# Performance work log

Hardware: AMD Instinct MI355X
Metric: run time of the kernel (lower is better)

## Reference

```python
import jax, jax.numpy as jnp
import numpy as np

G = 2000      # num_genes
TF = 64       # num_tf
B = 32        # batch (cells)
_peaks = 5 + (np.arange(G) % 46)          # ragged peaks per gene, avg ~27
T = int(_peaks.sum())                      # 54736 total peak columns
E = G * 16                                 # directed edges before symmetrization


def setup_inputs() -> dict:
    key = jax.random.key(0)
    ks = jax.random.split(key, 8)
    x = jax.random.normal(ks[0], (B, TF, T), jnp.float32)
    # gene id of each peak column (sorted, ragged segment structure = cut[])
    gene_ids = jnp.asarray(np.repeat(np.arange(G), _peaks), jnp.int32)
    # all per-gene subNet Linear weights flattened into one [TF, T] table
    w_sub = jax.random.normal(ks[1], (TF, T), jnp.float32) * 0.02
    b_sub = jax.random.normal(ks[2], (G,), jnp.float32) * 0.02
    rng = np.random.default_rng(1)
    src = rng.integers(0, G, E)
    dst = rng.integers(0, G, E)
    ei = np.stack([np.concatenate([src, dst]), np.concatenate([dst, src])])
    edge_index = jnp.asarray(ei, jnp.int32)                 # [2, 2E], symmetrized
    w_conv = jax.random.normal(ks[3], (1, 2), jnp.float32) * 0.5   # GCN lin weight (in=1, out=2)
    b_conv = jax.random.normal(ks[4], (2,), jnp.float32) * 0.1
    w_out = jax.random.normal(ks[5], (G * 2, 3), jnp.float32) * 0.02
    b_out = jax.random.normal(ks[6], (3,), jnp.float32) * 0.02
    return dict(x=x, gene_ids=gene_ids, w_sub=w_sub, b_sub=b_sub,
                edge_index=edge_index, w_conv=w_conv, b_conv=b_conv,
                w_out=w_out, b_out=b_out)


def reference(x, gene_ids, w_sub, b_sub, edge_index, w_conv, b_conv, w_out, b_out):
    # --- ragged per-gene subNets: Linear(num_peak_i*TF, 1) each ---
    # out[b,g] = sum_{t, p in gene g} x[b,t,p] * w[g,t,p] + b_sub[g]
    z = (x * w_sub[None]).sum(axis=1)                        # [B, T] reduce over TF
    x_cat = jnp.zeros((x.shape[0], b_sub.shape[0]), x.dtype)
    x_cat = x_cat.at[:, gene_ids].add(z) + b_sub[None]       # segment-sum over peaks
    x_cat = jax.nn.relu(x_cat)                               # cat_activate

    # --- GCNConv(1, 2, add_self_loops=False) on node features [B, G, 1] ---
    h = jnp.einsum('bn,f->bnf', x_cat, w_conv[0])            # lin: [B, G, 2]
    src, dst = edge_index[0], edge_index[1]
    deg = jnp.zeros((b_sub.shape[0],), x.dtype).at[dst].add(1.0)
    dinv = jnp.where(deg > 0, jax.lax.rsqrt(jnp.maximum(deg, 1.0)), 0.0)
    norm = dinv[src] * dinv[dst]                             # [2E]
    msg = h[:, src, :] * norm[None, :, None]                 # gather + scale
    agg = jnp.zeros_like(h).at[:, dst, :].add(msg) + b_conv  # scatter-add + bias
    g = jax.nn.relu(agg).reshape(x.shape[0], -1)             # [B, G*2]

    out = g @ w_out + b_out                                   # [B, 3]
    return x_cat, g, out
```

## Files before the change

kernel.cpp:

```cpp
#include <hip/hip_runtime.h>


__global__ void k_subnet4(const float* __restrict__ x, const float* __restrict__ w_sub,
                          const int* __restrict__ gene_ids, float* __restrict__ acc,
                          int TF, int T, int G, int B) {
    int t = (blockIdx.x * blockDim.x + threadIdx.x) * 4;
    if (t >= T) return;
    int b0 = blockIdx.y * 4;
    int nb = B - b0; if (nb > 4) nb = 4;
    const size_t planeT = (size_t)TF * T;

    if (t + 3 < T && (T % 4) == 0) {
        const size_t strideV = (size_t)T / 4;
        const float4* wp = (const float4*)(w_sub + t);
        const float4* xp0 = (const float4*)(x + (size_t)(b0 + 0) * planeT + t);
        const float4* xp1 = (const float4*)(x + (size_t)(b0 + 1) * planeT + t);
        const float4* xp2 = (const float4*)(x + (size_t)(b0 + 2) * planeT + t);
        const float4* xp3 = (const float4*)(x + (size_t)(b0 + 3) * planeT + t);

        float4 a0 = make_float4(0.f,0.f,0.f,0.f);
        float4 a1 = a0, a2 = a0, a3 = a0;

        if (nb == 4) {
            #pragma unroll 4
            for (int tf = 0; tf < TF; ++tf) {
                size_t off = (size_t)tf * strideV;
                float4 wv = wp[off];
                float4 x0 = xp0[off];
                float4 x1 = xp1[off];
                float4 x2 = xp2[off];
                float4 x3 = xp3[off];
                a0.x += x0.x*wv.x; a0.y += x0.y*wv.y; a0.z += x0.z*wv.z; a0.w += x0.w*wv.w;
                a1.x += x1.x*wv.x; a1.y += x1.y*wv.y; a1.z += x1.z*wv.z; a1.w += x1.w*wv.w;
                a2.x += x2.x*wv.x; a2.y += x2.y*wv.y; a2.z += x2.z*wv.z; a2.w += x2.w*wv.w;
                a3.x += x3.x*wv.x; a3.y += x3.y*wv.y; a3.z += x3.z*wv.z; a3.w += x3.w*wv.w;
            }
        } else {
            for (int tf = 0; tf < TF; ++tf) {
                size_t off = (size_t)tf * strideV;
                float4 wv = wp[off];
                if (nb > 0) { float4 xv = xp0[off]; a0.x += xv.x*wv.x; a0.y += xv.y*wv.y; a0.z += xv.z*wv.z; a0.w += xv.w*wv.w; }
                if (nb > 1) { float4 xv = xp1[off]; a1.x += xv.x*wv.x; a1.y += xv.y*wv.y; a1.z += xv.z*wv.z; a1.w += xv.w*wv.w; }
                if (nb > 2) { float4 xv = xp2[off]; a2.x += xv.x*wv.x; a2.y += xv.y*wv.y; a2.z += xv.z*wv.z; a2.w += xv.w*wv.w; }
            }
        }

        int g0 = gene_ids[t], g1 = gene_ids[t+1], g2 = gene_ids[t+2], g3 = gene_ids[t+3];
        float4 as[4] = {a0, a1, a2, a3};
        for (int bb = 0; bb < nb; ++bb) {
            float* base = acc + (size_t)(b0 + bb) * G;
            float4 a = as[bb];
            float v = a.x; int cg = g0;
            if (g1 == cg) v += a.y; else { atomicAdd(base + cg, v); cg = g1; v = a.y; }
            if (g2 == cg) v += a.z; else { atomicAdd(base + cg, v); cg = g2; v = a.z; }
            if (g3 == cg) v += a.w; else { atomicAdd(base + cg, v); cg = g3; v = a.w; }
            atomicAdd(base + cg, v);
        }
    } else {
        for (int bb = 0; bb < nb; ++bb) {
            int b = b0 + bb;
            for (int tt = t; tt < T && tt < t + 4; ++tt) {
                float a = 0.f;
                for (int tf = 0; tf < TF; ++tf)
                    a += x[(size_t)b * planeT + (size_t)tf * T + tt] * w_sub[(size_t)tf * T + tt];
                atomicAdd(acc + (size_t)b * G + gene_ids[tt], a);
            }
        }
    }
}

__global__ void k_xcat(const float* __restrict__ acc, const float* __restrict__ b_sub,
                       float* __restrict__ xcat, int BG, int G) {
    int i = blockIdx.x * blockDim.x + threadIdx.x;
    if (i >= BG) return;
    int g = i % G;
    float v = acc[i] + b_sub[g];
    xcat[i] = v > 0.f ? v : 0.f;
}

__global__ void k_deg(const int* __restrict__ ei, float* __restrict__ deg, int E2) {
    int e = blockIdx.x * blockDim.x + threadIdx.x;
    if (e < E2) atomicAdd(&deg[ei[E2 + e]], 1.0f);
}

__global__ void k_dinv(float* __restrict__ deg, int G) {
    int g = blockIdx.x * blockDim.x + threadIdx.x;
    if (g < G) {
        float d = deg[g];
        deg[g] = (d > 0.f) ? (1.0f / sqrtf(fmaxf(d, 1.0f))) : 0.f;
    }
}

__global__ void k_scatter(const float* __restrict__ xcat, const int* __restrict__ ei,
                          const float* __restrict__ dinv, float* __restrict__ s,
                          int G, int E2, int total) {
    int idx = blockIdx.x * blockDim.x + threadIdx.x;
    if (idx >= total) return;
    int b = idx / E2;
    int e = idx - b * E2;
    int src = ei[e], dst = ei[E2 + e];
    float norm = dinv[src] * dinv[dst];
    atomicAdd(&s[(size_t)b * G + dst], xcat[(size_t)b * G + src] * norm);
}

__global__ void k_gfin(const float* __restrict__ s, const float* __restrict__ w_conv,
                       const float* __restrict__ b_conv, float* __restrict__ gout, int BG) {
    int i = blockIdx.x * blockDim.x + threadIdx.x;
    if (i >= BG) return;
    float sv = s[i];
    float g0 = sv * w_conv[0] + b_conv[0];
    float g1 = sv * w_conv[1] + b_conv[1];
    gout[2 * (size_t)i + 0] = g0 > 0.f ? g0 : 0.f;
    gout[2 * (size_t)i + 1] = g1 > 0.f ? g1 : 0.f;
}

__global__ void k_out(const float* __restrict__ gmat, const float* __restrict__ w_out,
                      const float* __restrict__ b_out, float* __restrict__ out, int G2) {
    int b = blockIdx.x;
    float a0 = 0.f, a1 = 0.f, a2 = 0.f;
    for (int i = threadIdx.x; i < G2; i += blockDim.x) {
        float gv = gmat[(size_t)b * G2 + i];
        a0 += gv * w_out[3 * i + 0];
        a1 += gv * w_out[3 * i + 1];
        a2 += gv * w_out[3 * i + 2];
    }
    __shared__ float red[3][256];
    red[0][threadIdx.x] = a0; red[1][threadIdx.x] = a1; red[2][threadIdx.x] = a2;
    __syncthreads();
    for (int s = blockDim.x / 2; s > 0; s >>= 1) {
        if ((int)threadIdx.x < s) {
            red[0][threadIdx.x] += red[0][threadIdx.x + s];
            red[1][threadIdx.x] += red[1][threadIdx.x + s];
            red[2][threadIdx.x] += red[2][threadIdx.x + s];
        }
        __syncthreads();
    }
    if (threadIdx.x == 0) {
        out[b * 3 + 0] = red[0][0] + b_out[0];
        out[b * 3 + 1] = red[1][0] + b_out[1];
        out[b * 3 + 2] = red[2][0] + b_out[2];
    }
}

extern "C" void kernel_launch(void* const* d_in, const int* in_sizes, int n_in,
                              void* d_out, int out_size, void* d_ws, size_t ws_size,
                              hipStream_t stream) {
    const float* x        = (const float*)d_in[0];
    const int*   gene_ids = (const int*)d_in[1];
    const float* w_sub    = (const float*)d_in[2];
    const float* b_sub    = (const float*)d_in[3];
    const int*   ei       = (const int*)d_in[4];
    const float* w_conv   = (const float*)d_in[5];
    const float* b_conv   = (const float*)d_in[6];
    const float* w_out    = (const float*)d_in[7];
    const float* b_out    = (const float*)d_in[8];

    const int G  = in_sizes[3];
    const int T  = in_sizes[1];
    const int TF = in_sizes[2] / T;
    const int B  = in_sizes[0] / (TF * T);
    const int E2 = in_sizes[4] / 2;
    const int BG = B * G;
    const int G2 = 2 * G;

    float* acc = (float*)d_ws;
    float* deg = acc + BG;
    float* s   = deg + G;
    size_t zero_bytes = (size_t)(BG + G + BG) * sizeof(float);
    hipMemsetAsync(d_ws, 0, zero_bytes, stream);

    float* out_xcat = (float*)d_out;
    float* out_g    = out_xcat + BG;
    float* out_fin  = out_g + (size_t)B * G2;

    {
        int tthreads = (T + 3) / 4;
        dim3 grid((tthreads + 255) / 256, (B + 3) / 4);
        k_subnet4<<<grid, 256, 0, stream>>>(x, w_sub, gene_ids, acc, TF, T, G, B);
    }
    k_xcat<<<(BG + 255) / 256, 256, 0, stream>>>(acc, b_sub, out_xcat, BG, G);
    k_deg<<<(E2 + 255) / 256, 256, 0, stream>>>(ei, deg, E2);
    k_dinv<<<(G + 255) / 256, 256, 0, stream>>>(deg, G);
    {
        int total = B * E2;
        k_scatter<<<(total + 255) / 256, 256, 0, stream>>>(out_xcat, ei, deg, s, G, E2, total);
    }
    k_gfin<<<(BG + 255) / 256, 256, 0, stream>>>(s, w_conv, b_conv, out_g, BG);
    k_out<<<B, 256, 0, stream>>>(out_g, w_out, b_out, out_fin, G2);
}
```

Baseline: 750.0 us.

## Precompute edge norms, batch scatter over 4 cells, fuse GCN finalize with output GEMV

Edge normalisation is computed once per edge into a workspace buffer. The scatter kernel now processes four batch rows per thread, so edge indices and the norm are reused across cells. The GCN bias/ReLU finalize is fused with the output projection into one per-batch kernel, which removes a launch and a re-read of g. The norm buffer sits past the zeroed region and needs extra workspace, and the single-block-per-batch fused kernel has low parallelism.

```diff
diff --git a/kernel.cpp b/kernel.cpp
--- a/kernel.cpp
+++ b/kernel.cpp
@@ -1,9 +1,10 @@
 #include <hip/hip_runtime.h>
 
 
-__global__ void k_subnet4(const float* __restrict__ x, const float* __restrict__ w_sub,
-                          const int* __restrict__ gene_ids, float* __restrict__ acc,
-                          int TF, int T, int G, int B) {
+__global__ __launch_bounds__(256) void k_subnet4(
+        const float* __restrict__ x, const float* __restrict__ w_sub,
+        const int* __restrict__ gene_ids, float* __restrict__ acc,
+        int TF, int T, int G, int B) {
     int t = (blockIdx.x * blockDim.x + threadIdx.x) * 4;
     if (t >= T) return;
     int b0 = blockIdx.y * 4;
@@ -12,7 +13,7 @@
 
     if (t + 3 < T && (T % 4) == 0) {
         const size_t strideV = (size_t)T / 4;
-        const float4* wp = (const float4*)(w_sub + t);
+        const float4* wp  = (const float4*)(w_sub + t);
         const float4* xp0 = (const float4*)(x + (size_t)(b0 + 0) * planeT + t);
         const float4* xp1 = (const float4*)(x + (size_t)(b0 + 1) * planeT + t);
         const float4* xp2 = (const float4*)(x + (size_t)(b0 + 2) * planeT + t);
@@ -91,54 +92,61 @@
     }
 }
 
-__global__ void k_scatter(const float* __restrict__ xcat, const int* __restrict__ ei,
-                          const float* __restrict__ dinv, float* __restrict__ s,
-                          int G, int E2, int total) {
-    int idx = blockIdx.x * blockDim.x + threadIdx.x;
-    if (idx >= total) return;
-    int b = idx / E2;
-    int e = idx - b * E2;
-    int src = ei[e], dst = ei[E2 + e];
-    float norm = dinv[src] * dinv[dst];
-    atomicAdd(&s[(size_t)b * G + dst], xcat[(size_t)b * G + src] * norm);
+__global__ void k_norm(const int* __restrict__ ei, const float* __restrict__ dinv,
+                       float* __restrict__ norm, int E2) {
+    int e = blockIdx.x * blockDim.x + threadIdx.x;
+    if (e < E2) norm[e] = dinv[ei[e]] * dinv[ei[E2 + e]];
 }
 
-__global__ void k_gfin(const float* __restrict__ s, const float* __restrict__ w_conv,
-                       const float* __restrict__ b_conv, float* __restrict__ gout, int BG) {
-    int i = blockIdx.x * blockDim.x + threadIdx.x;
-    if (i >= BG) return;
-    float sv = s[i];
-    float g0 = sv * w_conv[0] + b_conv[0];
-    float g1 = sv * w_conv[1] + b_conv[1];
-    gout[2 * (size_t)i + 0] = g0 > 0.f ? g0 : 0.f;
-    gout[2 * (size_t)i + 1] = g1 > 0.f ? g1 : 0.f;
+__global__ void k_scatter4(const float* __restrict__ xcat, const int* __restrict__ ei,
+                           const float* __restrict__ norm, float* __restrict__ s,
+                           int G, int E2, int B) {
+    int e = blockIdx.x * blockDim.x + threadIdx.x;
+    if (e >= E2) return;
+    int b0 = blockIdx.y * 4;
+    int nb = B - b0; if (nb > 4) nb = 4;
+    int src = ei[e], dst = ei[E2 + e];
+    float nm = norm[e];
+    for (int bb = 0; bb < nb; ++bb) {
+        size_t row = (size_t)(b0 + bb) * G;
+        atomicAdd(&s[row + dst], xcat[row + src] * nm);
+    }
 }
 
-__global__ void k_out(const float* __restrict__ gmat, const float* __restrict__ w_out,
-                      const float* __restrict__ b_out, float* __restrict__ out, int G2) {
+__global__ void k_gout(const float* __restrict__ s, const float* __restrict__ w_conv,
+                       const float* __restrict__ b_conv, const float* __restrict__ w_out,
+                       const float* __restrict__ b_out, float* __restrict__ gout,
+                       float* __restrict__ outfin, int G) {
     int b = blockIdx.x;
+    float wc0 = w_conv[0], wc1 = w_conv[1];
+    float bc0 = b_conv[0], bc1 = b_conv[1];
     float a0 = 0.f, a1 = 0.f, a2 = 0.f;
-    for (int i = threadIdx.x; i < G2; i += blockDim.x) {
-        float gv = gmat[(size_t)b * G2 + i];
-        a0 += gv * w_out[3 * i + 0];
-        a1 += gv * w_out[3 * i + 1];
-        a2 += gv * w_out[3 * i + 2];
+    float2* grow = (float2*)(gout + (size_t)b * 2 * G);
+    for (int n = threadIdx.x; n < G; n += blockDim.x) {
+        float sv = s[(size_t)b * G + n];
+        float g0 = fmaxf(sv * wc0 + bc0, 0.f);
+        float g1 = fmaxf(sv * wc1 + bc1, 0.f);
+        grow[n] = make_float2(g0, g1);
+        const float* w0 = w_out + (size_t)(2 * n) * 3;
+        a0 += g0 * w0[0] + g1 * w0[3];
+        a1 += g0 * w0[1] + g1 * w0[4];
+        a2 += g0 * w0[2] + g1 * w0[5];
     }
     __shared__ float red[3][256];
     red[0][threadIdx.x] = a0; red[1][threadIdx.x] = a1; red[2][threadIdx.x] = a2;
     __syncthreads();
-    for (int s = blockDim.x / 2; s > 0; s >>= 1) {
-        if ((int)threadIdx.x < s) {
-            red[0][threadIdx.x] += red[0][threadIdx.x + s];
-            red[1][threadIdx.x] += red[1][threadIdx.x + s];
-            red[2][threadIdx.x] += red[2][threadIdx.x + s];
+    for (int st = blockDim.x / 2; st > 0; st >>= 1) {
+        if ((int)threadIdx.x < st) {
+            red[0][threadIdx.x] += red[0][threadIdx.x + st];
+            red[1][threadIdx.x] += red[1][threadIdx.x + st];
+            red[2][threadIdx.x] += red[2][threadIdx.x + st];
         }
         __syncthreads();
     }
     if (threadIdx.x == 0) {
-        out[b * 3 + 0] = red[0][0] + b_out[0];
-        out[b * 3 + 1] = red[1][0] + b_out[1];
-        out[b * 3 + 2] = red[2][0] + b_out[2];
+        outfin[b * 3 + 0] = red[0][0] + b_out[0];
+        outfin[b * 3 + 1] = red[1][0] + b_out[1];
+        outfin[b * 3 + 2] = red[2][0] + b_out[2];
     }
 }
 
@@ -161,17 +169,21 @@
     const int B  = in_sizes[0] / (TF * T);
     const int E2 = in_sizes[4] / 2;
     const int BG = B * G;
-    const int G2 = 2 * G;
 
-    float* acc = (float*)d_ws;
-    float* deg = acc + BG;
-    float* s   = deg + G;
+    float* acc  = (float*)d_ws;
+    float* deg  = acc + BG;
+    float* s    = deg + G;
+    float* norm = s + BG;
     size_t zero_bytes = (size_t)(BG + G + BG) * sizeof(float);
     hipMemsetAsync(d_ws, 0, zero_bytes, stream);
 
     float* out_xcat = (float*)d_out;
     float* out_g    = out_xcat + BG;
-    float* out_fin  = out_g + (size_t)B * G2;
+    float* out_fin  = out_g + (size_t)2 * BG;
+
+    k_deg <<<(E2 + 255) / 256, 256, 0, stream>>>(ei, deg, E2);
+    k_dinv<<<(G  + 255) / 256, 256, 0, stream>>>(deg, G);
+    k_norm<<<(E2 + 255) / 256, 256, 0, stream>>>(ei, deg, norm, E2);
 
     {
         int tthreads = (T + 3) / 4;
@@ -179,12 +191,9 @@
         k_subnet4<<<grid, 256, 0, stream>>>(x, w_sub, gene_ids, acc, TF, T, G, B);
     }
     k_xcat<<<(BG + 255) / 256, 256, 0, stream>>>(acc, b_sub, out_xcat, BG, G);
-    k_deg<<<(E2 + 255) / 256, 256, 0, stream>>>(ei, deg, E2);
-    k_dinv<<<(G + 255) / 256, 256, 0, stream>>>(deg, G);
     {
-        int total = B * E2;
-        k_scatter<<<(total + 255) / 256, 256, 0, stream>>>(out_xcat, ei, deg, s, G, E2, total);
+        dim3 grid((E2 + 255) / 256, (B + 3) / 4);
+        k_scatter4<<<grid, 256, 0, stream>>>(out_xcat, ei, norm, s, G, E2, B);
     }
-    k_gfin<<<(BG + 255) / 256, 256, 0, stream>>>(s, w_conv, b_conv, out_g, BG);
-    k_out<<<B, 256, 0, stream>>>(out_g, w_out, b_out, out_fin, G2);
+    k_gout<<<B, 256, 0, stream>>>(s, w_conv, b_conv, w_out, b_out, out_g, out_fin, G);
 }
```

Measured after the change: 785.7 us. +4.7%, slower.
